# Kernel tuning notes

Measured on AMD Instinct MI355X. Metric: run time of the kernel, lower is better.

The kernel has to match this reference:

```python
import jax, jax.numpy as jnp
import numpy as np

B, S, D, H = 2, 2048, 1024, 16
DH = D // H
DFF = 4 * D
EPS = 1e-5


def layernorm(x, g, b):
    mu = jnp.mean(x, axis=-1, keepdims=True)
    var = jnp.mean(jnp.square(x - mu), axis=-1, keepdims=True)
    return (x - mu) * jax.lax.rsqrt(var + EPS) * g + b


def setup_inputs() -> dict:
    key = jax.random.key(0)
    ks = jax.random.split(key, 12)
    s = 0.02
    return {
        "x": jax.random.normal(ks[0], (B, S, D), dtype=jnp.float32),
        "ln1_g": jnp.ones((D,), jnp.float32),
        "ln1_b": jnp.zeros((D,), jnp.float32),
        "Wq": jax.random.normal(ks[1], (D, D), jnp.float32) * s,
        "bq": jnp.zeros((D,), jnp.float32),
        "Wk": jax.random.normal(ks[2], (D, D), jnp.float32) * s,
        "bk": jnp.zeros((D,), jnp.float32),
        "Wv": jax.random.normal(ks[3], (D, D), jnp.float32) * s,
        "bv": jnp.zeros((D,), jnp.float32),
        "Wo": jax.random.normal(ks[4], (D, D), jnp.float32) * s,
        "bo": jnp.zeros((D,), jnp.float32),
        "ln2_g": jnp.ones((D,), jnp.float32),
        "ln2_b": jnp.zeros((D,), jnp.float32),
        "W1": jax.random.normal(ks[5], (D, DFF), jnp.float32) * s,
        "b1": jnp.zeros((DFF,), jnp.float32),
        "W2": jax.random.normal(ks[6], (DFF, D), jnp.float32) * s,
        "b2": jnp.zeros((D,), jnp.float32),
    }


def block(x, ln1_g, ln1_b, Wq, bq, Wk, bk, Wv, bv, Wo, bo, ln2_g, ln2_b, W1, b1, W2, b2):
    h = layernorm(x, ln1_g, ln1_b)
    # projections -> [B, H, S, DH]
    q = (h @ Wq + bq).reshape(B, S, H, DH).transpose(0, 2, 1, 3)
    k = (h @ Wk + bk).reshape(B, S, H, DH).transpose(0, 2, 1, 3)
    v = (h @ Wv + bv).reshape(B, S, H, DH).transpose(0, 2, 1, 3)
    scores = jnp.einsum('bhqd,bhkd->bhqk', q, k) / jnp.sqrt(jnp.float32(DH))
    causal = jnp.tril(jnp.ones((S, S), dtype=bool))  # True = keep
    scores = jnp.where(causal, scores, -jnp.inf)
    attn = jax.nn.softmax(scores, axis=-1)
    out = jnp.einsum('bhqk,bhkd->bhqd', attn, v)
    out = out.transpose(0, 2, 1, 3).reshape(B, S, D)
    x = x + out @ Wo + bo
    h2 = layernorm(x, ln2_g, ln2_b)
    ff = jax.nn.gelu(h2 @ W1 + b1, approximate=False) @ W2 + b2
    return x + ff


def reference(x, ln1_g, ln1_b, Wq, bq, Wk, bk, Wv, bv, Wo, bo, ln2_g, ln2_b, W1, b1, W2, b2):
    return block(x, ln1_g, ln1_b, Wq, bq, Wk, bk, Wv, bv, Wo, bo, ln2_g, ln2_b, W1, b1, W2, b2)
```

## Files before the change

kernel.cpp:

```cpp
#include <hip/hip_runtime.h>
#include <cstdint>
#include <cstddef>


#define DEV static __device__ __forceinline__

typedef unsigned short u16;
typedef __bf16 bf16x8 __attribute__((ext_vector_type(8)));
typedef u16    u16x8  __attribute__((ext_vector_type(8)));
typedef u16    u16x4  __attribute__((ext_vector_type(4)));
typedef float  f32x4  __attribute__((ext_vector_type(4)));

#define AEXP2(x) __builtin_amdgcn_exp2f(x)

DEV u16 f2bfh(float f) {
  return __builtin_bit_cast(u16, (__bf16)f);
}

DEV void gl16(const void* g, void* l) {
  __builtin_amdgcn_global_load_lds(
      (const __attribute__((address_space(1))) unsigned*)g,
      (__attribute__((address_space(3))) unsigned*)l, 16, 0, 0);
}

__global__ __launch_bounds__(256)
void tconv(const float* __restrict__ in, u16* __restrict__ out, int R, int C)
{
  __shared__ float tile[32][33];
  const int tx = threadIdx.x & 31, ty = threadIdx.x >> 5;
  const int r0 = blockIdx.y * 32, c0 = blockIdx.x * 32;
#pragma unroll
  for (int i = 0; i < 4; ++i)
    tile[ty + 8*i][tx] = in[(size_t)(r0 + ty + 8*i) * C + c0 + tx];
  __syncthreads();
#pragma unroll
  for (int i = 0; i < 4; ++i)
    out[(size_t)(c0 + ty + 8*i) * R + r0 + tx] = f2bfh(tile[tx][ty + 8*i]);
}

__global__ __launch_bounds__(256)
void tconv4(const float* __restrict__ w0, const float* __restrict__ w1,
            const float* __restrict__ w2, const float* __restrict__ w3,
            u16* __restrict__ q0, u16* __restrict__ q1,
            u16* __restrict__ q2, u16* __restrict__ q3)
{
  __shared__ float tile[32][33];
  const int z = blockIdx.z;
  const float* in = z == 0 ? w0 : z == 1 ? w1 : z == 2 ? w2 : w3;
  u16* out       = z == 0 ? q0 : z == 1 ? q1 : z == 2 ? q2 : q3;
  const int tx = threadIdx.x & 31, ty = threadIdx.x >> 5;
  const int r0 = blockIdx.y * 32, c0 = blockIdx.x * 32;
#pragma unroll
  for (int i = 0; i < 4; ++i)
    tile[ty + 8*i][tx] = in[(size_t)(r0 + ty + 8*i) * 1024 + c0 + tx];
  __syncthreads();
#pragma unroll
  for (int i = 0; i < 4; ++i)
    out[(size_t)(c0 + ty + 8*i) * 1024 + r0 + tx] = f2bfh(tile[tx][ty + 8*i]);
}

__global__ __launch_bounds__(256)
void ln_fwd(const float* __restrict__ x, const float* __restrict__ g,
            const float* __restrict__ b, u16* __restrict__ out)
{
  const int row = blockIdx.x, t = threadIdx.x;
  const float4 v = ((const float4*)(x + (size_t)row * 1024))[t];
  float s1 = v.x + v.y + v.z + v.w;
  float s2 = v.x*v.x + v.y*v.y + v.z*v.z + v.w*v.w;
#pragma unroll
  for (int d = 1; d < 64; d <<= 1) {
    s1 += __shfl_xor(s1, d, 64);
    s2 += __shfl_xor(s2, d, 64);
  }
  __shared__ float sh[8];
  const int w = t >> 6;
  if ((t & 63) == 0) { sh[w] = s1; sh[w + 4] = s2; }
  __syncthreads();
  s1 = sh[0] + sh[1] + sh[2] + sh[3];
  s2 = sh[4] + sh[5] + sh[6] + sh[7];
  const float mu  = s1 * (1.0f / 1024.0f);
  const float var = s2 * (1.0f / 1024.0f) - mu * mu;
  const float rs  = rsqrtf(var + 1e-5f);
  const float4 gv = ((const float4*)g)[t];
  const float4 bv = ((const float4*)b)[t];
  u16x4 o;
  o[0] = f2bfh((v.x - mu) * rs * gv.x + bv.x);
  o[1] = f2bfh((v.y - mu) * rs * gv.y + bv.y);
  o[2] = f2bfh((v.z - mu) * rs * gv.z + bv.z);
  o[3] = f2bfh((v.w - mu) * rs * gv.w + bv.w);
  *(u16x4*)(out + (size_t)row * 1024 + t * 4) = o;
}

#define EPI_QKV  0
#define EPI_RES  1
#define EPI_GELU 2

#define QSCALE 0.180421f

template<int EPI>
__global__ __launch_bounds__(512, 2)
void gemm256(const u16* __restrict__ A, const u16* __restrict__ Bt,
             const float* __restrict__ b0, const float* __restrict__ b1,
             const float* __restrict__ b2,
             u16* __restrict__ o0, u16* __restrict__ o1, u16* __restrict__ o2,
             int N, int K)
{
  __shared__ u16 As[2][256 * 64];
  __shared__ u16 Bs[2][256 * 64];
  const int t = threadIdx.x, lane = t & 63, w = t >> 6;
  const int wr = w >> 2, wc = w & 3;
  const int d = blockIdx.x + gridDim.x * blockIdx.y;
  const int rr = d >> 3;
  const int m0 = ((d & 7) * 2 + (rr & 1)) * 256;
  const int n0 = (rr >> 1) * 256;
  const int li = lane & 15, lg = lane >> 4;

  const int srow = t >> 3;
  const int schunk = (t & 7) ^ (srow & 7);
  const u16* Ag = A  + (size_t)(m0 + srow) * K + schunk * 8;
  const u16* Bg = Bt + (size_t)(n0 + srow) * K + schunk * 8;

  auto STG = [&](int k0, int b) {
#pragma unroll
    for (int p = 0; p < 4; ++p)
      gl16(Ag + k0 + (size_t)(p * 64) * K, &As[b][t * 8 + p * 4096]);
#pragma unroll
    for (int p = 0; p < 4; ++p)
      gl16(Bg + k0 + (size_t)(p * 64) * K, &Bs[b][t * 8 + p * 4096]);
  };

  f32x4 acc[8][4] = {};
  const int swz = (li & 7) << 4;

  auto COMPUTE = [&](int cur) {
#pragma unroll
    for (int ks = 0; ks < 2; ++ks) {
      bf16x8 af[8], bfr[4];
#pragma unroll
      for (int i = 0; i < 8; ++i) {
        const int Ra = wr * 128 + i * 16 + li;
        af[i] = *(const bf16x8*)((const char*)As[cur] + Ra * 128 +
                                 ((ks * 64 + lg * 16) ^ swz));
      }
#pragma unroll
      for (int i = 0; i < 4; ++i) {
        const int Rb = wc * 64 + i * 16 + li;
        bfr[i] = *(const bf16x8*)((const char*)Bs[cur] + Rb * 128 +
                                  ((ks * 64 + lg * 16) ^ swz));
      }
#pragma unroll
      for (int mi = 0; mi < 8; ++mi)
#pragma unroll
        for (int ni = 0; ni < 4; ++ni)
          acc[mi][ni] = __builtin_amdgcn_mfma_f32_16x16x32_bf16(
              af[mi], bfr[ni], acc[mi][ni], 0, 0, 0);
    }
  };

  STG(0, 0);
  for (int k0 = 0; k0 < K; k0 += 64) {
    const int cur = (k0 >> 6) & 1;
    if (k0 + 64 < K) {
      STG(k0 + 64, cur ^ 1);
      asm volatile("s_waitcnt vmcnt(8)" ::: "memory");
    } else {
      asm volatile("s_waitcnt vmcnt(0)" ::: "memory");
    }
    __builtin_amdgcn_s_barrier();
    __builtin_amdgcn_sched_barrier(0);
    COMPUTE(cur);
    __builtin_amdgcn_sched_barrier(0);
    __builtin_amdgcn_s_barrier();
  }

  const int crow = wr * 128 + lg * 4;
  const int ccol = wc * 64 + li;

  if (EPI == EPI_QKV) {
    const int which = n0 >> 10;
    const float* bias = which == 0 ? b0 : which == 1 ? b1 : b2;
    const int nn0 = n0 & 1023;
    if (which == 2) {
#pragma unroll
      for (int mi = 0; mi < 8; ++mi)
#pragma unroll
        for (int ni = 0; ni < 4; ++ni) {
          const int gm0 = m0 + crow + mi * 16;
          const int b_ = gm0 >> 11, s_ = gm0 & 2047;
          const int gc = nn0 + ccol + ni * 16;
          const int h_ = gc >> 6, d_ = gc & 63;
          u16x4 pk;
#pragma unroll
          for (int r = 0; r < 4; ++r) pk[r] = f2bfh(acc[mi][ni][r] + bias[gc]);
          *(u16x4*)(o2 + ((size_t)(b_ * 16 + h_) * 64 + d_) * 2048 + s_) = pk;
        }
    } else {
      u16* outp = which == 0 ? o0 : o1;
      const float sc = which == 0 ? QSCALE : 1.0f;
#pragma unroll
      for (int mi = 0; mi < 8; ++mi)
#pragma unroll
        for (int ni = 0; ni < 4; ++ni)
#pragma unroll
          for (int r = 0; r < 4; ++r) {
            const int gm = m0 + crow + mi * 16 + r;
            const int gc = nn0 + ccol + ni * 16;
            const float v = (acc[mi][ni][r] + bias[gc]) * sc;
            const int b_ = gm >> 11, s_ = gm & 2047;
            const int h_ = gc >> 6,  d_ = gc & 63;
            outp[((size_t)(b_ * 16 + h_) * 2048 + s_) * 64 + d_] = f2bfh(v);
          }
    }
  } else {
#pragma unroll
    for (int mi = 0; mi < 8; ++mi)
#pragma unroll
      for (int ni = 0; ni < 4; ++ni)
#pragma unroll
        for (int r = 0; r < 4; ++r) {
          const int gm = m0 + crow + mi * 16 + r;
          const int gn = n0 + ccol + ni * 16;
          const float v = acc[mi][ni][r] + b0[gn];
          const float y = 0.7978845608f * (v + 0.044715f * v * v * v);
          const float e = AEXP2(fminf(y * 2.8853900818f, 80.0f));
          const float gl = v * e * __builtin_amdgcn_rcpf(e + 1.0f);
          o0[(size_t)gm * N + gn] = f2bfh(gl);
        }
  }
}

template<int EPI, int BM, int CM>
__global__ __launch_bounds__(256)
void gemm_bt(const u16* __restrict__ A, const u16* __restrict__ Bt,
             const float* __restrict__ b0, const float* __restrict__ res,
             float* __restrict__ outf, u16* __restrict__ o0,
             int N, int K)
{
  constexpr int MI = BM / 32;
  constexpr int RA = BM / 32;
  static_assert(BM == 64, "vmcnt(6) assumes 6 loads/step");
  __shared__ u16 As[3][BM * 64];
  __shared__ u16 Bs[3][128 * 64];
  const int t = threadIdx.x, lane = t & 63, w = t >> 6;
  const int wr = w >> 1, wc = w & 1;
  const int d = blockIdx.x + gridDim.x * blockIdx.y;
  const int rr = d >> 3;
  const int m0 = ((d & 7) * CM + rr % CM) * BM;
  const int n0 = (rr / CM) * 128;
  const int li = lane & 15, lg = lane >> 4;

  const int srow = t >> 3;
  const int schunk = (t & 7) ^ (srow & 7);
  const u16* Ag = A  + (size_t)(m0 + srow) * K + schunk * 8;
  const u16* Bg = Bt + (size_t)(n0 + srow) * K + schunk * 8;

  auto STG = [&](int k0, int b) {
#pragma unroll
    for (int p = 0; p < RA; ++p)
      gl16(Ag + k0 + (size_t)(p * 32) * K, &As[b][t * 8 + p * 2048]);
#pragma unroll
    for (int p = 0; p < 4; ++p)
      gl16(Bg + k0 + (size_t)(p * 32) * K, &Bs[b][t * 8 + p * 2048]);
  };

  f32x4 acc[MI][4] = {};
  const int swz = (li & 7) << 4;

  auto COMPUTE = [&](int cur) {
#pragma unroll
    for (int ks = 0; ks < 2; ++ks) {
      bf16x8 af[MI], bfr[4];
#pragma unroll
      for (int i = 0; i < MI; ++i) {
        const int Ra = wr * (MI * 16) + i * 16 + li;
        af[i] = *(const bf16x8*)((const char*)As[cur] + Ra * 128 +
                                 ((ks * 64 + lg * 16) ^ swz));
      }
#pragma unroll
      for (int i = 0; i < 4; ++i) {
        const int Rb = wc * 64 + i * 16 + li;
        bfr[i] = *(const bf16x8*)((const char*)Bs[cur] + Rb * 128 +
                                  ((ks * 64 + lg * 16) ^ swz));
      }
#pragma unroll
      for (int mi = 0; mi < MI; ++mi)
#pragma unroll
        for (int ni = 0; ni < 4; ++ni)
          acc[mi][ni] = __builtin_amdgcn_mfma_f32_16x16x32_bf16(
              af[mi], bfr[ni], acc[mi][ni], 0, 0, 0);
    }
  };

  STG(0, 0);
  if (64 < K) STG(64, 1);
  int cur = 0;
  for (int k0 = 0; k0 < K; k0 += 64) {
    if (k0 + 64 < K)
      asm volatile("s_waitcnt vmcnt(6)" ::: "memory");
    else
      asm volatile("s_waitcnt vmcnt(0)" ::: "memory");
    __builtin_amdgcn_s_barrier();
    __builtin_amdgcn_sched_barrier(0);
    COMPUTE(cur);
    if (k0 + 128 < K) {
      int nxt = cur + 2; if (nxt >= 3) nxt -= 3;
      STG(k0 + 128, nxt);
    }
    cur = (cur + 1 == 3) ? 0 : cur + 1;
  }

  const int crow = wr * (MI * 16) + lg * 4;
  const int ccol = wc * 64 + li;
#pragma unroll
  for (int mi = 0; mi < MI; ++mi)
#pragma unroll
    for (int ni = 0; ni < 4; ++ni)
#pragma unroll
      for (int r = 0; r < 4; ++r) {
        const int gm = m0 + crow + mi * 16 + r;
        const int gn = n0 + ccol + ni * 16;
        const float v = acc[mi][ni][r] + b0[gn];
        const size_t o = (size_t)gm * N + gn;
        outf[o] = v + res[o];
      }
}

__global__ __launch_bounds__(512, 4)
void attn_fwd(const u16* __restrict__ qb, const u16* __restrict__ kb,
              const u16* __restrict__ vtb, u16* __restrict__ ob)
{
  __shared__ u16 Ks[2][128 * 64];
  __shared__ u16 Vt[2][64 * 128];
  __shared__ u16 Ps[8][16 * 64];
  const int t = threadIdx.x, w = t >> 6, lane = t & 63;
  const int li = lane & 15, lg = lane >> 4;
  const int bh = blockIdx.y;
  const int bx = blockIdx.x;
  const int qt = (bh & 16) ? (15 - bx) : bx;
  const int q0 = qt * 128;

  const size_t qrow = (size_t)bh * 2048 + q0 + w * 16 + li;
  const bf16x8 aq0 = *(const bf16x8*)(qb + qrow * 64 + lg * 8);
  const bf16x8 aq1 = *(const bf16x8*)(qb + qrow * 64 + lg * 8 + 32);

  f32x4 o[4] = {};
  float mrun[4], lrun[4];
#pragma unroll
  for (int r = 0; r < 4; ++r) { mrun[r] = -1e30f; lrun[r] = 0.0f; }

  const u16* kbase = kb  + (size_t)bh * 2048 * 64;
  const u16* vbase = vtb + (size_t)bh * 64 * 2048;
  const int ntile = qt + 1;

  const int kchunk = (t & 7)  ^ ((t >> 3) & 7);
  const int vchunk = (t & 15) ^ ((t >> 4) & 15);
  const u16* kg = kbase + (size_t)(t >> 3) * 64 + kchunk * 8;
  const u16* vg = vbase + (size_t)(t >> 4) * 2048 + vchunk * 8;

#define STAGE(tk_, b_)                                              \
  {                                                                 \
    const int kv0s = (tk_) * 128;                                   \
    gl16(kg + (size_t)kv0s * 64,        &Ks[b_][t * 8]);            \
    gl16(kg + (size_t)(kv0s + 64) * 64, &Ks[b_][t * 8 + 4096]);     \
    gl16(vg + kv0s,                     &Vt[b_][t * 8]);            \
    gl16(vg + kv0s + (size_t)32 * 2048, &Vt[b_][t * 8 + 4096]);     \
  }

  STAGE(0, 0);
  __syncthreads();

  for (int tk = 0; tk < ntile; ++tk) {
    const int cur = tk & 1;
    const int kv0 = tk * 128;
    if (tk + 1 < ntile) STAGE(tk + 1, 1 - cur);

    f32x4 s[8];
    __builtin_amdgcn_s_setprio(1);
#pragma unroll
    for (int cf = 0; cf < 8; ++cf) {
      const int row = cf * 16 + li;
      const char* kc = (const char*)Ks[cur] + row * 128;
      const int sw = (row & 7) << 4;
      const bf16x8 bk0 = *(const bf16x8*)(kc + ((lg * 16)      ^ sw));
      const bf16x8 bk1 = *(const bf16x8*)(kc + ((lg * 16 + 64) ^ sw));
      f32x4 z = {};
      z = __builtin_amdgcn_mfma_f32_16x16x32_bf16(aq0, bk0, z, 0, 0, 0);
      z = __builtin_amdgcn_mfma_f32_16x16x32_bf16(aq1, bk1, z, 0, 0, 0);
      s[cf] = z;
    }
    __builtin_amdgcn_s_setprio(0);
    const int row0 = q0 + w * 16 + lg * 4;
    if (tk == ntile - 1) {
#pragma unroll
      for (int cf = 0; cf < 8; ++cf)
#pragma unroll
        for (int r = 0; r < 4; ++r)
          if (kv0 + cf * 16 + li > row0 + r) s[cf][r] = -1e30f;
    }

    float pmax[4];
#pragma unroll
    for (int r = 0; r < 4; ++r) {
      const float a = fmaxf(fmaxf(s[0][r], s[1][r]), fmaxf(s[2][r], s[3][r]));
      const float b = fmaxf(fmaxf(s[4][r], s[5][r]), fmaxf(s[6][r], s[7][r]));
      pmax[r] = fmaxf(a, b);
    }
    bool need = false;
#pragma unroll
    for (int r = 0; r < 4; ++r) need = need || (pmax[r] > mrun[r] + 11.5f);
    if (__any((int)need)) {
#pragma unroll
      for (int d = 1; d < 16; d <<= 1)
#pragma unroll
        for (int r = 0; r < 4; ++r)
          pmax[r] = fmaxf(pmax[r], __shfl_xor(pmax[r], d, 64));
#pragma unroll
      for (int r = 0; r < 4; ++r) {
        const float mnew = fmaxf(mrun[r], pmax[r]);
        const float scl  = AEXP2(mrun[r] - mnew);
        lrun[r] *= scl;
#pragma unroll
        for (int n = 0; n < 4; ++n) o[n][r] *= scl;
        mrun[r] = mnew;
      }
    }
#pragma unroll
    for (int cf = 0; cf < 8; ++cf)
#pragma unroll
      for (int r = 0; r < 4; ++r) {
        const float pv = AEXP2(s[cf][r] - mrun[r]);
        s[cf][r] = pv;
        lrun[r] += pv;
      }

#pragma unroll
    for (int kh = 0; kh < 2; ++kh) {
#pragma unroll
      for (int cf2 = 0; cf2 < 4; ++cf2)
#pragma unroll
        for (int r = 0; r < 4; ++r) {
          const int prow = lg * 4 + r;
          const int pcolB = (cf2 * 16 + li) * 2;
          *(u16*)((char*)Ps[w] + prow * 128 + (pcolB ^ ((prow & 7) << 4))) =
              f2bfh(s[kh * 4 + cf2][r]);
        }
      __builtin_amdgcn_s_setprio(1);
#pragma unroll
      for (int ks = 0; ks < 2; ++ks) {
        const char* pc = (const char*)Ps[w] + li * 128;
        const bf16x8 ap =
            *(const bf16x8*)(pc + ((lg * 16 + ks * 64) ^ ((li & 7) << 4)));
#pragma unroll
        for (int n = 0; n < 4; ++n) {
          const int vrow = n * 16 + li;
          const char* vc = (const char*)Vt[cur] + vrow * 256;
          const int colB = lg * 16 + ks * 64 + kh * 128;
          const bf16x8 bv =
              *(const bf16x8*)(vc + (colB ^ ((vrow & 15) << 4)));
          o[n] = __builtin_amdgcn_mfma_f32_16x16x32_bf16(ap, bv, o[n], 0, 0, 0);
        }
      }
      __builtin_amdgcn_s_setprio(0);
    }

    __syncthreads();
  }
#undef STAGE

#pragma unroll
  for (int d = 1; d < 16; d <<= 1)
#pragma unroll
    for (int r = 0; r < 4; ++r)
      lrun[r] += __shfl_xor(lrun[r], d, 64);

  float inv[4];
#pragma unroll
  for (int r = 0; r < 4; ++r) inv[r] = __builtin_amdgcn_rcpf(lrun[r]);
  const int b_ = bh >> 4, h_ = bh & 15;
#pragma unroll
  for (int n = 0; n < 4; ++n)
#pragma unroll
    for (int r = 0; r < 4; ++r) {
      const int rowg = q0 + w * 16 + lg * 4 + r;
      ob[((size_t)b_ * 2048 + rowg) * 1024 + h_ * 64 + n * 16 + li] =
          f2bfh(o[n][r] * inv[r]);
    }
}

extern "C" void kernel_launch(void* const* d_in, const int* in_sizes, int n_in,
                              void* d_out, int out_size, void* d_ws, size_t ws_size,
                              hipStream_t stream) {
  const float* x    = (const float*)d_in[0];
  const float* ln1g = (const float*)d_in[1];
  const float* ln1b = (const float*)d_in[2];
  const float* Wq   = (const float*)d_in[3];
  const float* bq   = (const float*)d_in[4];
  const float* Wk   = (const float*)d_in[5];
  const float* bk   = (const float*)d_in[6];
  const float* Wv   = (const float*)d_in[7];
  const float* bv   = (const float*)d_in[8];
  const float* Wo   = (const float*)d_in[9];
  const float* bo   = (const float*)d_in[10];
  const float* ln2g = (const float*)d_in[11];
  const float* ln2b = (const float*)d_in[12];
  const float* W1   = (const float*)d_in[13];
  const float* b1   = (const float*)d_in[14];
  const float* W2   = (const float*)d_in[15];
  const float* b2   = (const float*)d_in[16];

  char* ws = (char*)d_ws;
  const size_t MB = 1u << 20;
  u16*   hb   = (u16*)(ws + 0);
  u16*   Wqt  = (u16*)(ws + 8  * MB);
  u16*   Wkt  = (u16*)(ws + 10 * MB);
  u16*   Wvt  = (u16*)(ws + 12 * MB);
  u16*   Wot  = (u16*)(ws + 14 * MB);
  u16*   W1t  = (u16*)(ws + 16 * MB);
  u16*   W2t  = (u16*)(ws + 24 * MB);
  u16*   qbuf = (u16*)(ws + 32 * MB);
  u16*   kbuf = (u16*)(ws + 40 * MB);
  u16*   aob  = (u16*)(ws + 48 * MB);
  u16*   vtb  = (u16*)(ws + 56 * MB);
  float* x2   = (float*)(ws + 64 * MB);
  u16*   h2   = hb;
  u16*   ff1  = qbuf;

  const dim3 blk(256);
  tconv4<<<dim3(32, 32, 4), blk, 0, stream>>>(Wq, Wk, Wv, Wo, Wqt, Wkt, Wvt, Wot);
  tconv<<<dim3(128, 32), blk, 0, stream>>>(W1, W1t, 1024, 4096);
  tconv<<<dim3(32, 128), blk, 0, stream>>>(W2, W2t, 4096, 1024);

  ln_fwd<<<4096, blk, 0, stream>>>(x, ln1g, ln1b, hb);

  gemm256<EPI_QKV><<<dim3(12, 16), dim3(512), 0, stream>>>(
      hb, Wqt, bq, bk, bv, qbuf, kbuf, vtb, 3072, 1024);

  attn_fwd<<<dim3(16, 32), dim3(512), 0, stream>>>(qbuf, kbuf, vtb, aob);

  gemm_bt<EPI_RES, 64, 8><<<dim3(8, 64), blk, 0, stream>>>(
      aob, Wot, bo, x, x2, nullptr, 1024, 1024);

  ln_fwd<<<4096, blk, 0, stream>>>(x2, ln2g, ln2b, h2);

  gemm256<EPI_GELU><<<dim3(16, 16), dim3(512), 0, stream>>>(
      h2, W1t, b1, nullptr, nullptr, ff1, nullptr, nullptr, 4096, 1024);

  gemm_bt<EPI_RES, 64, 8><<<dim3(8, 64), blk, 0, stream>>>(
      ff1, W2t, b2, x2, (float*)d_out, nullptr, 1024, 4096);
}
```

Baseline: 214.4 us.

## Triple-buffer GEMM with BK=32 tiles and interleaved staging inside compute

Reworks the 256x256 GEMM main loop from double-buffered BK=64 tiles to triple-buffered BK=32 tiles. Global-to-LDS loads for tile k+2 are issued between the two halves of the MFMA work, and the trailing barrier is dropped. The LDS layout and swizzle change to fit the 64-byte rows, and s_setprio raises wave priority around the MFMA bursts. The aim is more load/compute overlap and fewer barriers per unit of work. The cost is more loop iterations, a new swizzle whose bank-conflict behaviour is untested, and reliance on three buffers to make it safe to skip the end-of-iteration sync.

```diff
diff --git a/kernel.cpp b/kernel.cpp
--- a/kernel.cpp
+++ b/kernel.cpp
@@ -105,8 +105,8 @@
              u16* __restrict__ o0, u16* __restrict__ o1, u16* __restrict__ o2,
              int N, int K)
 {
-  __shared__ u16 As[2][256 * 64];
-  __shared__ u16 Bs[2][256 * 64];
+  __shared__ u16 As[3][8192];
+  __shared__ u16 Bs[3][8192];
   const int t = threadIdx.x, lane = t & 63, w = t >> 6;
   const int wr = w >> 2, wc = w & 3;
   const int d = blockIdx.x + gridDim.x * blockIdx.y;
@@ -115,62 +115,78 @@
   const int n0 = (rr >> 1) * 256;
   const int li = lane & 15, lg = lane >> 4;
 
-  const int srow = t >> 3;
-  const int schunk = (t & 7) ^ (srow & 7);
-  const u16* Ag = A  + (size_t)(m0 + srow) * K + schunk * 8;
-  const u16* Bg = Bt + (size_t)(n0 + srow) * K + schunk * 8;
-
-  auto STG = [&](int k0, int b) {
-#pragma unroll
-    for (int p = 0; p < 4; ++p)
-      gl16(Ag + k0 + (size_t)(p * 64) * K, &As[b][t * 8 + p * 4096]);
-#pragma unroll
-    for (int p = 0; p < 4; ++p)
-      gl16(Bg + k0 + (size_t)(p * 64) * K, &Bs[b][t * 8 + p * 4096]);
+  const int srow = t >> 2;
+  const int skc  = (t & 3) ^ ((t >> 3) & 3);
+  const u16* Ag = A  + (size_t)(m0 + srow) * K + skc * 8;
+  const u16* Bg = Bt + (size_t)(n0 + srow) * K + skc * 8;
+
+  auto STG_A = [&](int k0, int b) {
+#pragma unroll
+    for (int p = 0; p < 2; ++p)
+      gl16(Ag + k0 + (size_t)(p * 128) * K, &As[b][t * 8 + p * 4096]);
   };
+  auto STG_B = [&](int k0, int b) {
+#pragma unroll
+    for (int p = 0; p < 2; ++p)
+      gl16(Bg + k0 + (size_t)(p * 128) * K, &Bs[b][t * 8 + p * 4096]);
+  };
+
+  auto ldsoff = [](int R, int kc) {
+    return (R >> 1) * 128 + (R & 1) * 64 + ((kc ^ ((R >> 1) & 3)) << 4);
+  };
 
   f32x4 acc[8][4] = {};
-  const int swz = (li & 7) << 4;
-
-  auto COMPUTE = [&](int cur) {
-#pragma unroll
-    for (int ks = 0; ks < 2; ++ks) {
-      bf16x8 af[8], bfr[4];
-#pragma unroll
-      for (int i = 0; i < 8; ++i) {
-        const int Ra = wr * 128 + i * 16 + li;
-        af[i] = *(const bf16x8*)((const char*)As[cur] + Ra * 128 +
-                                 ((ks * 64 + lg * 16) ^ swz));
-      }
-#pragma unroll
-      for (int i = 0; i < 4; ++i) {
-        const int Rb = wc * 64 + i * 16 + li;
-        bfr[i] = *(const bf16x8*)((const char*)Bs[cur] + Rb * 128 +
-                                  ((ks * 64 + lg * 16) ^ swz));
-      }
-#pragma unroll
-      for (int mi = 0; mi < 8; ++mi)
-#pragma unroll
-        for (int ni = 0; ni < 4; ++ni)
-          acc[mi][ni] = __builtin_amdgcn_mfma_f32_16x16x32_bf16(
-              af[mi], bfr[ni], acc[mi][ni], 0, 0, 0);
-    }
-  };
-
-  STG(0, 0);
-  for (int k0 = 0; k0 < K; k0 += 64) {
-    const int cur = (k0 >> 6) & 1;
-    if (k0 + 64 < K) {
-      STG(k0 + 64, cur ^ 1);
-      asm volatile("s_waitcnt vmcnt(8)" ::: "memory");
-    } else {
+  const int NT = K >> 5;
+
+  STG_A(0, 0);  STG_B(0, 0);
+  STG_A(32, 1); STG_B(32, 1);
+
+  int cur = 0, nxt = 2;
+  for (int kt = 0; kt < NT; ++kt) {
+    if (kt + 1 < NT)
+      asm volatile("s_waitcnt vmcnt(4)" ::: "memory");
+    else
       asm volatile("s_waitcnt vmcnt(0)" ::: "memory");
-    }
     __builtin_amdgcn_s_barrier();
     __builtin_amdgcn_sched_barrier(0);
-    COMPUTE(cur);
-    __builtin_amdgcn_sched_barrier(0);
-    __builtin_amdgcn_s_barrier();
+
+    const int k2 = (kt + 2) * 32;
+    bf16x8 bfr[4], afA[4];
+#pragma unroll
+    for (int i = 0; i < 4; ++i)
+      bfr[i] = *(const bf16x8*)((const char*)Bs[cur] +
+                                ldsoff(wc * 64 + i * 16 + li, lg));
+#pragma unroll
+    for (int i = 0; i < 4; ++i)
+      afA[i] = *(const bf16x8*)((const char*)As[cur] +
+                                ldsoff(wr * 128 + i * 16 + li, lg));
+    if (kt + 2 < NT) STG_A(k2, nxt);
+    __builtin_amdgcn_s_setprio(1);
+#pragma unroll
+    for (int mi = 0; mi < 4; ++mi)
+#pragma unroll
+      for (int ni = 0; ni < 4; ++ni)
+        acc[mi][ni] = __builtin_amdgcn_mfma_f32_16x16x32_bf16(
+            afA[mi], bfr[ni], acc[mi][ni], 0, 0, 0);
+    __builtin_amdgcn_s_setprio(0);
+
+    bf16x8 afB[4];
+#pragma unroll
+    for (int i = 0; i < 4; ++i)
+      afB[i] = *(const bf16x8*)((const char*)As[cur] +
+                                ldsoff(wr * 128 + (4 + i) * 16 + li, lg));
+    if (kt + 2 < NT) STG_B(k2, nxt);
+    __builtin_amdgcn_s_setprio(1);
+#pragma unroll
+    for (int mi = 0; mi < 4; ++mi)
+#pragma unroll
+      for (int ni = 0; ni < 4; ++ni)
+        acc[4 + mi][ni] = __builtin_amdgcn_mfma_f32_16x16x32_bf16(
+            afB[mi], bfr[ni], acc[4 + mi][ni], 0, 0, 0);
+    __builtin_amdgcn_s_setprio(0);
+
+    cur = (cur + 1 == 3) ? 0 : cur + 1;
+    nxt = (nxt + 1 == 3) ? 0 : nxt + 1;
   }
 
   const int crow = wr * 128 + lg * 4;
```

Result: faster. 207.4 us (-3.2%).
